# Optimization experiments

Hardware: AMD Instinct MI355X
Metric: run time of the kernel (lower is better)

Reference implementation:

```python
import jax, jax.numpy as jnp
import numpy as np

V, E, HD, K = 100000, 128, 256, 9
B, T = 128, 512
H = HD // 2  # per-direction hidden size


def setup_inputs() -> dict:
    key = jax.random.key(0)
    ks = jax.random.split(key, 16)
    s = 0.1
    rn = lambda k, shape: jax.random.normal(k, shape, jnp.float32) * s
    sentences = jax.random.randint(ks[0], (B, T), 0, V, dtype=jnp.int32)
    lengths = jax.random.randint(ks[1], (B,), 1, T + 1, dtype=jnp.int32)
    return {
        'sentences': sentences,
        'lengths': lengths,
        'embed': rn(ks[2], (V, E)),
        'Wih_f': rn(ks[3], (4 * H, E)), 'Whh_f': rn(ks[4], (4 * H, H)),
        'bih_f': rn(ks[5], (4 * H,)), 'bhh_f': rn(ks[6], (4 * H,)),
        'Wih_b': rn(ks[7], (4 * H, E)), 'Whh_b': rn(ks[8], (4 * H, H)),
        'bih_b': rn(ks[9], (4 * H,)), 'bhh_b': rn(ks[10], (4 * H,)),
        'W_out': rn(ks[11], (K, HD)), 'b_out': rn(ks[12], (K,)),
        'start_t': rn(ks[13], (K,)), 'end_t': rn(ks[14], (K,)),
        'trans': rn(ks[15], (K, K)),
    }


def _lstm(x, mask, Wih, Whh, bih, bhh, reverse):
    # x: [B,T,E], mask: [B,T] bool. Replicates packed-sequence semantics:
    # state frozen and output zeroed at padding positions (padding is trailing,
    # so reverse=True starts fresh at each sequence's true end).
    Bv, Hv = x.shape[0], Whh.shape[1]
    bias = bih + bhh

    def step(carry, inp):
        h, c = carry
        x_t, m_t = inp  # [B,E], [B,1]
        gates = x_t @ Wih.T + h @ Whh.T + bias  # [B,4H]
        i, f, g, o = jnp.split(gates, 4, axis=-1)  # torch gate order i,f,g,o
        c_new = jax.nn.sigmoid(f) * c + jax.nn.sigmoid(i) * jnp.tanh(g)
        h_new = jax.nn.sigmoid(o) * jnp.tanh(c_new)
        h = jnp.where(m_t, h_new, h)
        c = jnp.where(m_t, c_new, c)
        return (h, c), h * m_t.astype(h.dtype)

    init = (jnp.zeros((Bv, Hv), x.dtype), jnp.zeros((Bv, Hv), x.dtype))
    xs = (jnp.swapaxes(x, 0, 1), jnp.swapaxes(mask, 0, 1)[..., None])
    _, hs = jax.lax.scan(step, init, xs, reverse=reverse)
    return jnp.swapaxes(hs, 0, 1)  # [B,T,H]


def _emissions(sentences, mask, embed, Wih_f, Whh_f, bih_f, bhh_f,
               Wih_b, Whh_b, bih_b, bhh_b, W_out, b_out):
    x = embed[sentences]  # [B,T,E] (dropout is identity at inference)
    hf = _lstm(x, mask, Wih_f, Whh_f, bih_f, bhh_f, reverse=False)
    hb = _lstm(x, mask, Wih_b, Whh_b, bih_b, bhh_b, reverse=True)
    h = jnp.concatenate([hf, hb], axis=-1)  # [B,T,2H]
    return jnp.einsum('btd,kd->btk', h, W_out) + b_out  # [B,T,K]


def _viterbi(em, mask, start_t, end_t, trans):
    # torchcrf-style batched Viterbi decode. em: [B,T,K], mask: [B,T] bool.
    Kv = em.shape[-1]
    ident = jnp.arange(Kv, dtype=jnp.int32)[None]  # identity backpointers for pads
    score0 = start_t[None] + em[:, 0]  # [B,K]

    def step(score, inp):
        em_t, m_t = inp  # [B,K], [B,1]
        cand = score[:, :, None] + trans[None] + em_t[:, None, :]  # [B,K_prev,K_cur]
        new_score = cand.max(axis=1)
        idx = cand.argmax(axis=1).astype(jnp.int32)  # [B,K]
        score = jnp.where(m_t, new_score, score)
        idx = jnp.where(m_t, idx, ident)
        return score, idx

    xs = (jnp.swapaxes(em[:, 1:], 0, 1), jnp.swapaxes(mask[:, 1:], 0, 1)[..., None])
    score, hist = jax.lax.scan(step, score0, xs)  # hist: [T-1,B,K]
    score = score + end_t[None]
    last_tag = jnp.argmax(score, axis=-1).astype(jnp.int32)  # [B]

    def back(tag, idx_t):
        prev = jnp.take_along_axis(idx_t, tag[:, None], axis=1)[:, 0]
        return prev, prev

    _, tags_prev = jax.lax.scan(back, last_tag, hist, reverse=True)  # [T-1,B]
    tags = jnp.swapaxes(jnp.concatenate([tags_prev, last_tag[None]], axis=0), 0, 1)
    return jnp.where(mask, tags, 0), score.max(axis=-1)


def reference(sentences, lengths, embed, Wih_f, Whh_f, bih_f, bhh_f,
              Wih_b, Whh_b, bih_b, bhh_b, W_out, b_out, start_t, end_t, trans):
    mask = jnp.arange(sentences.shape[1])[None] < lengths[:, None]  # [B,T]
    em = _emissions(sentences, mask, embed, Wih_f, Whh_f, bih_f, bhh_f,
                    Wih_b, Whh_b, bih_b, bhh_b, W_out, b_out)
    tags, _ = _viterbi(em, mask, start_t, end_t, trans)
    return tags  # [B,T] int32, padded positions set to 0
```

## Files before the change

### kernel.cpp

```cpp
#include <hip/hip_runtime.h>
#include <cmath>

#define B_  128
#define T_  512
#define E_  128
#define H_  128
#define G4  512
#define K_  9

__global__ __launch_bounds__(256, 2)
void proj_gemm(const int* __restrict__ sent, const float* __restrict__ embed,
               const float* __restrict__ Wf, const float* __restrict__ Wb,
               const float* __restrict__ bif, const float* __restrict__ bhf,
               const float* __restrict__ bib, const float* __restrict__ bhb,
               float* __restrict__ proj, int t0f, int Tc)
{
  __shared__ __align__(16) float Al[128 * 64];
  __shared__ __align__(16) float Bl[128 * 64];
  const int tid   = threadIdx.x;
  const int ntile = blockIdx.x;
  const int mtile = blockIdx.y;
  const int tpb   = Tc >> 6;
  const int b     = mtile / tpb;
  const int toff  = (mtile - b * tpb) << 6;
  const int dir   = ntile >> 3;
  const int t0    = dir ? (T_ - t0f - Tc) : t0f;
  const float* __restrict__ W = dir ? Wb : Wf;
  const int n0 = (ntile & 7) << 6;

  {
    const int r  = tid & 63;
    const int kc = tid >> 6;
    const int t  = t0 + toff + r;
    const int vid = sent[b * T_ + t];
    const float* arow = embed + (size_t)vid * E_ + kc * 32;
    const float* brow = W + (size_t)(n0 + r) * E_ + kc * 32;
#pragma unroll
    for (int q = 0; q < 8; ++q) {
      float4 av = *(const float4*)(arow + q * 4);
      float4 bv = *(const float4*)(brow + q * 4);
      int k0 = kc * 32 + q * 4;
      Al[(k0 + 0) * 64 + r] = av.x; Al[(k0 + 1) * 64 + r] = av.y;
      Al[(k0 + 2) * 64 + r] = av.z; Al[(k0 + 3) * 64 + r] = av.w;
      Bl[(k0 + 0) * 64 + r] = bv.x; Bl[(k0 + 1) * 64 + r] = bv.y;
      Bl[(k0 + 2) * 64 + r] = bv.z; Bl[(k0 + 3) * 64 + r] = bv.w;
    }
  }
  __syncthreads();

  const int mg = tid & 15, ng = tid >> 4;
  float acc[4][4] = {};
#pragma unroll 8
  for (int k = 0; k < 128; ++k) {
    float4 a  = *(const float4*)&Al[k * 64 + mg * 4];
    float4 bb = *(const float4*)&Bl[k * 64 + ng * 4];
    acc[0][0] += a.x * bb.x; acc[0][1] += a.x * bb.y; acc[0][2] += a.x * bb.z; acc[0][3] += a.x * bb.w;
    acc[1][0] += a.y * bb.x; acc[1][1] += a.y * bb.y; acc[1][2] += a.y * bb.z; acc[1][3] += a.y * bb.w;
    acc[2][0] += a.z * bb.x; acc[2][1] += a.z * bb.y; acc[2][2] += a.z * bb.z; acc[2][3] += a.z * bb.w;
    acc[3][0] += a.w * bb.x; acc[3][1] += a.w * bb.y; acc[3][2] += a.w * bb.z; acc[3][3] += a.w * bb.w;
  }

  const float* bi = dir ? bib : bif;
  const float* bh = dir ? bhb : bhf;
  const int nl = ng * 4;
  float4 bias;
  bias.x = bi[n0 + nl + 0] + bh[n0 + nl + 0];
  bias.y = bi[n0 + nl + 1] + bh[n0 + nl + 1];
  bias.z = bi[n0 + nl + 2] + bh[n0 + nl + 2];
  bias.w = bi[n0 + nl + 3] + bh[n0 + nl + 3];
#pragma unroll
  for (int i = 0; i < 4; ++i) {
    const int tloc = toff + mg * 4 + i;
    float4 o;
    o.x = acc[i][0] + bias.x; o.y = acc[i][1] + bias.y;
    o.z = acc[i][2] + bias.z; o.w = acc[i][3] + bias.w;
    *(float4*)&proj[((size_t)(b * Tc + tloc)) * 1024 + dir * G4 + n0 + nl] = o;
  }
}

__global__ __launch_bounds__(512, 1)
void lstm_chunk(const float* __restrict__ proj,
                const float* __restrict__ Whf, const float* __restrict__ Whb,
                const int* __restrict__ lengths,
                float* __restrict__ hs,
                float* __restrict__ sh, float* __restrict__ sc,
                int t0f, int Tc, int first)
{
  const int dir = blockIdx.x;
  const int b   = blockIdx.y;
  const int tid = threadIdx.x;
  const float* __restrict__ Whh = dir ? Whb : Whf;
  __shared__ __align__(16) float h_lds[H_];
  __shared__ float gates[G4];

  float w[128];
  {
    const float* wr = Whh + (size_t)tid * H_;
#pragma unroll
    for (int k = 0; k < 128; k += 4) {
      float4 v = *(const float4*)(wr + k);
      w[k] = v.x; w[k + 1] = v.y; w[k + 2] = v.z; w[k + 3] = v.w;
    }
  }
#pragma unroll
  for (int k = 0; k < 128; ++k) asm volatile("" : "+v"(w[k]));

  const int len = lengths[b];
  const int t0  = dir ? (T_ - t0f - Tc) : t0f;
  float c = 0.f;
  if (tid < H_) {
    if (first) {
      h_lds[tid] = 0.f;
    } else {
      h_lds[tid] = sh[(dir * B_ + b) * H_ + tid];
      c          = sc[(dir * B_ + b) * H_ + tid];
    }
  }
  __syncthreads();

  const float* projp = proj + (size_t)b * Tc * 1024 + dir * G4 + tid;
  float pv = projp[(size_t)(dir ? (Tc - 1) : 0) * 1024];
  for (int s = 0; s < Tc; ++s) {
    const int tc = dir ? (Tc - 1 - s) : s;
    const int t  = t0 + tc;
    float nv = 0.f;
    if (s + 1 < Tc) {
      const int tcn = dir ? (Tc - 2 - s) : (s + 1);
      nv = projp[(size_t)tcn * 1024];
    }
    float a0 = 0.f, a1 = 0.f, a2 = 0.f, a3 = 0.f;
#pragma unroll
    for (int k4 = 0; k4 < 32; ++k4) {
      float4 h4 = *(const float4*)&h_lds[k4 * 4];
      a0 += w[4 * k4 + 0] * h4.x; a1 += w[4 * k4 + 1] * h4.y;
      a2 += w[4 * k4 + 2] * h4.z; a3 += w[4 * k4 + 3] * h4.w;
    }
    float acc = pv + (a0 + a1) + (a2 + a3);
    const int blk = tid >> 7;
    gates[tid] = (blk == 2) ? tanhf(acc) : 1.f / (1.f + expf(-acc));
    __syncthreads();
    if (tid < H_) {
      float gi = gates[tid], gf = gates[tid + 128];
      float gg = gates[tid + 256], go = gates[tid + 384];
      float cn = gf * c + gi * gg;
      float hn = go * tanhf(cn);
      bool  m  = (t < len);
      float hold = h_lds[tid];
      c = m ? cn : c;
      h_lds[tid] = m ? hn : hold;
      hs[(size_t)(b * T_ + t) * 256 + dir * H_ + tid] = m ? hn : 0.f;
    }
    __syncthreads();
    pv = nv;
  }
  if (tid < H_) {
    sh[(dir * B_ + b) * H_ + tid] = h_lds[tid];
    sc[(dir * B_ + b) * H_ + tid] = c;
  }
}

__global__ __launch_bounds__(256)
void emis_kernel(const float* __restrict__ hs, const float* __restrict__ Wout,
                 const float* __restrict__ bout, float* __restrict__ em)
{
  __shared__ __align__(16) float Wl[K_ * 256];
  const int tid = threadIdx.x;
  for (int i = tid; i < K_ * 256; i += 256) Wl[i] = Wout[i];
  __syncthreads();
  const int m = blockIdx.x * 256 + tid;
  const float* h = hs + (size_t)m * 256;
  float acc[K_] = {};
#pragma unroll 4
  for (int kk = 0; kk < 64; ++kk) {
    float4 h4 = *(const float4*)(h + kk * 4);
#pragma unroll
    for (int k9 = 0; k9 < K_; ++k9) {
      float4 w4 = *(const float4*)&Wl[k9 * 256 + kk * 4];
      acc[k9] += h4.x * w4.x + h4.y * w4.y + h4.z * w4.z + h4.w * w4.w;
    }
  }
#pragma unroll
  for (int k9 = 0; k9 < K_; ++k9) em[(size_t)m * K_ + k9] = acc[k9] + bout[k9];
}

__global__ __launch_bounds__(64)
void viterbi_kernel(const float* __restrict__ em, const int* __restrict__ lengths,
                    const float* __restrict__ st, const float* __restrict__ en,
                    const float* __restrict__ trans, int* __restrict__ tags)
{
  const int b    = blockIdx.x;
  const int lane = threadIdx.x;
  __shared__ unsigned char hist[(T_ - 1) * 16];
  const int len = lengths[b];
  float tr[K_];
#pragma unroll
  for (int j = 0; j < K_; ++j) tr[j] = (lane < K_) ? trans[j * K_ + lane] : 0.f;
  float s = (lane < K_) ? st[lane] + em[(size_t)(b * T_) * K_ + lane] : -1e30f;
  for (int t = 1; t < len; ++t) {
    float best = -1e30f; int bj = 0;
#pragma unroll
    for (int j = 0; j < K_; ++j) {
      float v = __shfl(s, j) + tr[j];
      if (v > best) { best = v; bj = j; }
    }
    if (lane < K_) {
      s = best + em[(size_t)(b * T_ + t) * K_ + lane];
      hist[(t - 1) * 16 + lane] = (unsigned char)bj;
    }
  }
  float fs = (lane < K_) ? s + en[lane] : -1e30f;
  float best = -1e30f; int last = 0;
#pragma unroll
  for (int j = 0; j < K_; ++j) {
    float v = __shfl(fs, j);
    if (v > best) { best = v; last = j; }
  }
  __syncthreads();
  if (lane == 0) {
    int tag = last;
    tags[b * T_ + len - 1] = tag;
    for (int t = len - 2; t >= 0; --t) {
      tag = hist[t * 16 + tag];
      tags[b * T_ + t] = tag;
    }
  }
  for (int t = len + lane; t < T_; t += 64) tags[b * T_ + t] = 0;
}

extern "C" void kernel_launch(void* const* d_in, const int* in_sizes, int n_in,
                              void* d_out, int out_size, void* d_ws, size_t ws_size,
                              hipStream_t stream)
{
  const int*   sent  = (const int*)d_in[0];
  const int*   lens  = (const int*)d_in[1];
  const float* embed = (const float*)d_in[2];
  const float* Wif   = (const float*)d_in[3];
  const float* Whf   = (const float*)d_in[4];
  const float* bif   = (const float*)d_in[5];
  const float* bhf   = (const float*)d_in[6];
  const float* Wib   = (const float*)d_in[7];
  const float* Whb   = (const float*)d_in[8];
  const float* bib   = (const float*)d_in[9];
  const float* bhb   = (const float*)d_in[10];
  const float* Wout  = (const float*)d_in[11];
  const float* bout  = (const float*)d_in[12];
  const float* stt   = (const float*)d_in[13];
  const float* ent   = (const float*)d_in[14];
  const float* trans = (const float*)d_in[15];
  int* tags = (int*)d_out;

  float* ws   = (float*)d_ws;
  float* hs   = ws;
  float* em   = hs + (size_t)B_ * T_ * 256;
  float* sh   = em + (size_t)B_ * T_ * K_;
  float* sc   = sh + (size_t)2 * B_ * H_;
  float* proj = sc + (size_t)2 * B_ * H_;
  const size_t fixed_bytes = (size_t)(proj - ws) * sizeof(float);

  int Tc = 512;
  while (Tc > 64 && fixed_bytes + (size_t)B_ * Tc * 1024 * sizeof(float) > ws_size)
    Tc >>= 1;

  const int nch = T_ / Tc;
  for (int c2 = 0; c2 < nch; ++c2) {
    const int t0f = c2 * Tc;
    dim3 g1(16, B_ * (Tc >> 6));
    hipLaunchKernelGGL(proj_gemm, g1, dim3(256), 0, stream,
                       sent, embed, Wif, Wib, bif, bhf, bib, bhb, proj, t0f, Tc);
    dim3 g2(2, B_);
    hipLaunchKernelGGL(lstm_chunk, g2, dim3(512), 0, stream,
                       proj, Whf, Whb, lens, hs, sh, sc, t0f, Tc, (int)(c2 == 0));
  }
  hipLaunchKernelGGL(emis_kernel, dim3((B_ * T_) / 256), dim3(256), 0, stream,
                     hs, Wout, bout, em);
  hipLaunchKernelGGL(viterbi_kernel, dim3(B_), dim3(64), 0, stream,
                     em, lens, stt, ent, trans, tags);
}
```

Measured before the change: 967.8 us.

## Enlarge projection GEMM tile to 128x128 with 8x8 micro-tiles and double-buffered K

Reworks the embedding-gather input projection GEMM to use 128x128 output tiles with an 8x8 per-thread register micro-tile. K is staged in 32-wide slices through double-buffered shared memory, with the next slice loaded into registers while the current one is computed. This raises arithmetic intensity per shared-memory load and hides global-load latency. The cost is much higher register pressure (64 accumulators) and a minimum chunk size of 128.

Measured after the change: 2.838 ms. 193% more time.

```diff
diff --git a/kernel.cpp b/kernel.cpp
--- a/kernel.cpp
+++ b/kernel.cpp
@@ -15,66 +15,99 @@
                const float* __restrict__ bib, const float* __restrict__ bhb,
                float* __restrict__ proj, int t0f, int Tc)
 {
-  __shared__ __align__(16) float Al[128 * 64];
-  __shared__ __align__(16) float Bl[128 * 64];
+  __shared__ __align__(16) float Al[2][32][128];
+  __shared__ __align__(16) float Bl[2][32][128];
   const int tid   = threadIdx.x;
   const int ntile = blockIdx.x;
   const int mtile = blockIdx.y;
-  const int tpb   = Tc >> 6;
-  const int b     = mtile / tpb;
-  const int toff  = (mtile - b * tpb) << 6;
-  const int dir   = ntile >> 3;
+  const int dir   = ntile >> 2;
+  const int n0    = (ntile & 3) << 7;
   const int t0    = dir ? (T_ - t0f - Tc) : t0f;
   const float* __restrict__ W = dir ? Wb : Wf;
-  const int n0 = (ntile & 7) << 6;
-
-  {
-    const int r  = tid & 63;
-    const int kc = tid >> 6;
-    const int t  = t0 + toff + r;
-    const int vid = sent[b * T_ + t];
-    const float* arow = embed + (size_t)vid * E_ + kc * 32;
-    const float* brow = W + (size_t)(n0 + r) * E_ + kc * 32;
-#pragma unroll
-    for (int q = 0; q < 8; ++q) {
-      float4 av = *(const float4*)(arow + q * 4);
-      float4 bv = *(const float4*)(brow + q * 4);
-      int k0 = kc * 32 + q * 4;
-      Al[(k0 + 0) * 64 + r] = av.x; Al[(k0 + 1) * 64 + r] = av.y;
-      Al[(k0 + 2) * 64 + r] = av.z; Al[(k0 + 3) * 64 + r] = av.w;
-      Bl[(k0 + 0) * 64 + r] = bv.x; Bl[(k0 + 1) * 64 + r] = bv.y;
-      Bl[(k0 + 2) * 64 + r] = bv.z; Bl[(k0 + 3) * 64 + r] = bv.w;
-    }
-  }
-  __syncthreads();
+
+  const int row = tid & 127;
+  const int kh  = (tid >> 7) << 4;
+  const int mrow0 = mtile * 128 + row;
+  const int b   = mrow0 / Tc;
+  const int tc  = mrow0 - b * Tc;
+  const int vid = sent[b * T_ + t0 + tc];
+  const float* __restrict__ arow = embed + (size_t)vid * E_ + kh;
+  const float* __restrict__ brow = W + (size_t)(n0 + row) * E_ + kh;
+
+  float4 va[4], vb[4];
+#pragma unroll
+  for (int q = 0; q < 4; ++q) {
+    va[q] = *(const float4*)(arow + q * 4);
+    vb[q] = *(const float4*)(brow + q * 4);
+  }
+#pragma unroll
+  for (int q = 0; q < 4; ++q) {
+    const int k = kh + q * 4;
+    Al[0][k + 0][row] = va[q].x; Al[0][k + 1][row] = va[q].y;
+    Al[0][k + 2][row] = va[q].z; Al[0][k + 3][row] = va[q].w;
+    Bl[0][k + 0][row] = vb[q].x; Bl[0][k + 1][row] = vb[q].y;
+    Bl[0][k + 2][row] = vb[q].z; Bl[0][k + 3][row] = vb[q].w;
+  }
 
   const int mg = tid & 15, ng = tid >> 4;
-  float acc[4][4] = {};
-#pragma unroll 8
-  for (int k = 0; k < 128; ++k) {
-    float4 a  = *(const float4*)&Al[k * 64 + mg * 4];
-    float4 bb = *(const float4*)&Bl[k * 64 + ng * 4];
-    acc[0][0] += a.x * bb.x; acc[0][1] += a.x * bb.y; acc[0][2] += a.x * bb.z; acc[0][3] += a.x * bb.w;
-    acc[1][0] += a.y * bb.x; acc[1][1] += a.y * bb.y; acc[1][2] += a.y * bb.z; acc[1][3] += a.y * bb.w;
-    acc[2][0] += a.z * bb.x; acc[2][1] += a.z * bb.y; acc[2][2] += a.z * bb.z; acc[2][3] += a.z * bb.w;
-    acc[3][0] += a.w * bb.x; acc[3][1] += a.w * bb.y; acc[3][2] += a.w * bb.z; acc[3][3] += a.w * bb.w;
+  float acc[8][8] = {};
+
+  for (int s = 0; s < 4; ++s) {
+    __syncthreads();
+    if (s < 3) {
+      const int kb = (s + 1) * 32;
+#pragma unroll
+      for (int q = 0; q < 4; ++q) {
+        va[q] = *(const float4*)(arow + kb + q * 4);
+        vb[q] = *(const float4*)(brow + kb + q * 4);
+      }
+    }
+    const int bs = s & 1;
+#pragma unroll
+    for (int k = 0; k < 32; ++k) {
+      float4 a0 = *(const float4*)&Al[bs][k][mg * 4];
+      float4 a1 = *(const float4*)&Al[bs][k][64 + mg * 4];
+      float4 b0 = *(const float4*)&Bl[bs][k][ng * 4];
+      float4 b1 = *(const float4*)&Bl[bs][k][64 + ng * 4];
+      float av[8] = {a0.x, a0.y, a0.z, a0.w, a1.x, a1.y, a1.z, a1.w};
+      float bv[8] = {b0.x, b0.y, b0.z, b0.w, b1.x, b1.y, b1.z, b1.w};
+#pragma unroll
+      for (int i = 0; i < 8; ++i)
+#pragma unroll
+        for (int j = 0; j < 8; ++j) acc[i][j] += av[i] * bv[j];
+    }
+    if (s < 3) {
+      const int nb = (s + 1) & 1;
+#pragma unroll
+      for (int q = 0; q < 4; ++q) {
+        const int k = kh + q * 4;
+        Al[nb][k + 0][row] = va[q].x; Al[nb][k + 1][row] = va[q].y;
+        Al[nb][k + 2][row] = va[q].z; Al[nb][k + 3][row] = va[q].w;
+        Bl[nb][k + 0][row] = vb[q].x; Bl[nb][k + 1][row] = vb[q].y;
+        Bl[nb][k + 2][row] = vb[q].z; Bl[nb][k + 3][row] = vb[q].w;
+      }
+    }
   }
 
   const float* bi = dir ? bib : bif;
   const float* bh = dir ? bhb : bhf;
-  const int nl = ng * 4;
-  float4 bias;
-  bias.x = bi[n0 + nl + 0] + bh[n0 + nl + 0];
-  bias.y = bi[n0 + nl + 1] + bh[n0 + nl + 1];
-  bias.z = bi[n0 + nl + 2] + bh[n0 + nl + 2];
-  bias.w = bi[n0 + nl + 3] + bh[n0 + nl + 3];
-#pragma unroll
-  for (int i = 0; i < 4; ++i) {
-    const int tloc = toff + mg * 4 + i;
-    float4 o;
-    o.x = acc[i][0] + bias.x; o.y = acc[i][1] + bias.y;
-    o.z = acc[i][2] + bias.z; o.w = acc[i][3] + bias.w;
-    *(float4*)&proj[((size_t)(b * Tc + tloc)) * 1024 + dir * G4 + n0 + nl] = o;
+  float bias[8];
+#pragma unroll
+  for (int cj = 0; cj < 8; ++cj) {
+    const int col = n0 + (cj >> 2) * 64 + ng * 4 + (cj & 3);
+    bias[cj] = bi[col] + bh[col];
+  }
+#pragma unroll
+  for (int ri = 0; ri < 8; ++ri) {
+    const int mrow = mtile * 128 + (ri >> 2) * 64 + mg * 4 + (ri & 3);
+    float* prow = proj + (size_t)mrow * 1024 + dir * G4 + n0;
+    float4 o0, o1;
+    o0.x = acc[ri][0] + bias[0]; o0.y = acc[ri][1] + bias[1];
+    o0.z = acc[ri][2] + bias[2]; o0.w = acc[ri][3] + bias[3];
+    o1.x = acc[ri][4] + bias[4]; o1.y = acc[ri][5] + bias[5];
+    o1.z = acc[ri][6] + bias[6]; o1.w = acc[ri][7] + bias[7];
+    *(float4*)&prow[ng * 4]      = o0;
+    *(float4*)&prow[64 + ng * 4] = o1;
   }
 }
 
@@ -258,13 +291,13 @@
   const size_t fixed_bytes = (size_t)(proj - ws) * sizeof(float);
 
   int Tc = 512;
-  while (Tc > 64 && fixed_bytes + (size_t)B_ * Tc * 1024 * sizeof(float) > ws_size)
+  while (Tc > 128 && fixed_bytes + (size_t)B_ * Tc * 1024 * sizeof(float) > ws_size)
     Tc >>= 1;
 
   const int nch = T_ / Tc;
   for (int c2 = 0; c2 < nch; ++c2) {
     const int t0f = c2 * Tc;
-    dim3 g1(16, B_ * (Tc >> 6));
+    dim3 g1(8, (B_ * Tc) >> 7);
     hipLaunchKernelGGL(proj_gemm, g1, dim3(256), 0, stream,
                        sent, embed, Wif, Wib, bif, bhf, bib, bhb, proj, t0f, Tc);
     dim3 g2(2, B_);
```

## Retile projection GEMM to 128x128 blocks with 8x8 register microtiles

Applied to the files above, without the earlier changes.

The input-projection GEMM moves from 64x64 output tiles with a 4x4 per-thread microtile to 128x128 tiles with an 8x8 microtile. The K dimension is staged through LDS in two halves of 64. The goal is to raise arithmetic intensity per LDS and global load and cut the number of blocks. In exchange it uses more registers per thread, drops the 2-blocks-per-CU launch bound, and requires the time chunk Tc to be at least 128.

Measured after the change: 1.059 ms. +9.5%, slower.

```diff
diff --git a/kernel.cpp b/kernel.cpp
--- a/kernel.cpp
+++ b/kernel.cpp
@@ -8,73 +8,95 @@
 #define G4  512
 #define K_  9
 
-__global__ __launch_bounds__(256, 2)
+#define MT8(L, R, A)                                              \
+  L.x += A * B0.x; L.y += A * B0.y; L.z += A * B0.z; L.w += A * B0.w; \
+  R.x += A * B1.x; R.y += A * B1.y; R.z += A * B1.z; R.w += A * B1.w;
+
+__global__ __launch_bounds__(256)
 void proj_gemm(const int* __restrict__ sent, const float* __restrict__ embed,
                const float* __restrict__ Wf, const float* __restrict__ Wb,
                const float* __restrict__ bif, const float* __restrict__ bhf,
                const float* __restrict__ bib, const float* __restrict__ bhb,
                float* __restrict__ proj, int t0f, int Tc)
 {
-  __shared__ __align__(16) float Al[128 * 64];
-  __shared__ __align__(16) float Bl[128 * 64];
+  __shared__ __align__(16) float Al[64][128];
+  __shared__ __align__(16) float Bl[64][128];
   const int tid   = threadIdx.x;
   const int ntile = blockIdx.x;
   const int mtile = blockIdx.y;
-  const int tpb   = Tc >> 6;
-  const int b     = mtile / tpb;
-  const int toff  = (mtile - b * tpb) << 6;
-  const int dir   = ntile >> 3;
+  const int dir   = ntile >> 2;
+  const int n0    = (ntile & 3) << 7;
   const int t0    = dir ? (T_ - t0f - Tc) : t0f;
   const float* __restrict__ W = dir ? Wb : Wf;
-  const int n0 = (ntile & 7) << 6;
-
-  {
-    const int r  = tid & 63;
-    const int kc = tid >> 6;
-    const int t  = t0 + toff + r;
-    const int vid = sent[b * T_ + t];
-    const float* arow = embed + (size_t)vid * E_ + kc * 32;
-    const float* brow = W + (size_t)(n0 + r) * E_ + kc * 32;
+
+  const int row   = tid & 127;
+  const int kh    = (tid >> 7) << 5;
+  const int mrow0 = mtile * 128 + row;
+  const int b     = mrow0 / Tc;
+  const int tc    = mrow0 - b * Tc;
+  const int vid   = sent[b * T_ + t0 + tc];
+  const float* __restrict__ arow = embed + (size_t)vid * E_ + kh;
+  const float* __restrict__ brow = W + (size_t)(n0 + row) * E_ + kh;
+
+  const int mg = tid & 15, ng = tid >> 4;
+  float4 accL[8] = {}, accR[8] = {};
+  for (int s = 0; s < 2; ++s) {
+    if (s) __syncthreads();
+    const int kb = s << 6;
 #pragma unroll
     for (int q = 0; q < 8; ++q) {
-      float4 av = *(const float4*)(arow + q * 4);
-      float4 bv = *(const float4*)(brow + q * 4);
-      int k0 = kc * 32 + q * 4;
-      Al[(k0 + 0) * 64 + r] = av.x; Al[(k0 + 1) * 64 + r] = av.y;
-      Al[(k0 + 2) * 64 + r] = av.z; Al[(k0 + 3) * 64 + r] = av.w;
-      Bl[(k0 + 0) * 64 + r] = bv.x; Bl[(k0 + 1) * 64 + r] = bv.y;
-      Bl[(k0 + 2) * 64 + r] = bv.z; Bl[(k0 + 3) * 64 + r] = bv.w;
-    }
-  }
-  __syncthreads();
-
-  const int mg = tid & 15, ng = tid >> 4;
-  float acc[4][4] = {};
-#pragma unroll 8
-  for (int k = 0; k < 128; ++k) {
-    float4 a  = *(const float4*)&Al[k * 64 + mg * 4];
-    float4 bb = *(const float4*)&Bl[k * 64 + ng * 4];
-    acc[0][0] += a.x * bb.x; acc[0][1] += a.x * bb.y; acc[0][2] += a.x * bb.z; acc[0][3] += a.x * bb.w;
-    acc[1][0] += a.y * bb.x; acc[1][1] += a.y * bb.y; acc[1][2] += a.y * bb.z; acc[1][3] += a.y * bb.w;
-    acc[2][0] += a.z * bb.x; acc[2][1] += a.z * bb.y; acc[2][2] += a.z * bb.z; acc[2][3] += a.z * bb.w;
-    acc[3][0] += a.w * bb.x; acc[3][1] += a.w * bb.y; acc[3][2] += a.w * bb.z; acc[3][3] += a.w * bb.w;
+      float4 v = *(const float4*)(arow + kb + q * 4);
+      const int k = kh + q * 4;
+      Al[k + 0][row] = v.x; Al[k + 1][row] = v.y;
+      Al[k + 2][row] = v.z; Al[k + 3][row] = v.w;
+    }
+#pragma unroll
+    for (int q = 0; q < 8; ++q) {
+      float4 v = *(const float4*)(brow + kb + q * 4);
+      const int k = kh + q * 4;
+      Bl[k + 0][row] = v.x; Bl[k + 1][row] = v.y;
+      Bl[k + 2][row] = v.z; Bl[k + 3][row] = v.w;
+    }
+    __syncthreads();
+#pragma unroll
+    for (int k = 0; k < 64; ++k) {
+      float4 A0 = *(const float4*)&Al[k][mg * 4];
+      float4 A1 = *(const float4*)&Al[k][64 + mg * 4];
+      float4 B0 = *(const float4*)&Bl[k][ng * 4];
+      float4 B1 = *(const float4*)&Bl[k][64 + ng * 4];
+      MT8(accL[0], accR[0], A0.x)
+      MT8(accL[1], accR[1], A0.y)
+      MT8(accL[2], accR[2], A0.z)
+      MT8(accL[3], accR[3], A0.w)
+      MT8(accL[4], accR[4], A1.x)
+      MT8(accL[5], accR[5], A1.y)
+      MT8(accL[6], accR[6], A1.z)
+      MT8(accL[7], accR[7], A1.w)
+    }
   }
 
   const float* bi = dir ? bib : bif;
   const float* bh = dir ? bhb : bhf;
-  const int nl = ng * 4;
-  float4 bias;
-  bias.x = bi[n0 + nl + 0] + bh[n0 + nl + 0];
-  bias.y = bi[n0 + nl + 1] + bh[n0 + nl + 1];
-  bias.z = bi[n0 + nl + 2] + bh[n0 + nl + 2];
-  bias.w = bi[n0 + nl + 3] + bh[n0 + nl + 3];
-#pragma unroll
-  for (int i = 0; i < 4; ++i) {
-    const int tloc = toff + mg * 4 + i;
-    float4 o;
-    o.x = acc[i][0] + bias.x; o.y = acc[i][1] + bias.y;
-    o.z = acc[i][2] + bias.z; o.w = acc[i][3] + bias.w;
-    *(float4*)&proj[((size_t)(b * Tc + tloc)) * 1024 + dir * G4 + n0 + nl] = o;
+  float4 biasL, biasR;
+  biasL.x = bi[n0 + ng * 4 + 0] + bh[n0 + ng * 4 + 0];
+  biasL.y = bi[n0 + ng * 4 + 1] + bh[n0 + ng * 4 + 1];
+  biasL.z = bi[n0 + ng * 4 + 2] + bh[n0 + ng * 4 + 2];
+  biasL.w = bi[n0 + ng * 4 + 3] + bh[n0 + ng * 4 + 3];
+  biasR.x = bi[n0 + 64 + ng * 4 + 0] + bh[n0 + 64 + ng * 4 + 0];
+  biasR.y = bi[n0 + 64 + ng * 4 + 1] + bh[n0 + 64 + ng * 4 + 1];
+  biasR.z = bi[n0 + 64 + ng * 4 + 2] + bh[n0 + 64 + ng * 4 + 2];
+  biasR.w = bi[n0 + 64 + ng * 4 + 3] + bh[n0 + 64 + ng * 4 + 3];
+#pragma unroll
+  for (int i = 0; i < 8; ++i) {
+    const int mrow = mtile * 128 + (i >> 2) * 64 + mg * 4 + (i & 3);
+    float* prow = proj + (size_t)mrow * 1024 + dir * G4 + n0;
+    float4 oL, oR;
+    oL.x = accL[i].x + biasL.x; oL.y = accL[i].y + biasL.y;
+    oL.z = accL[i].z + biasL.z; oL.w = accL[i].w + biasL.w;
+    oR.x = accR[i].x + biasR.x; oR.y = accR[i].y + biasR.y;
+    oR.z = accR[i].z + biasR.z; oR.w = accR[i].w + biasR.w;
+    *(float4*)&prow[ng * 4]      = oL;
+    *(float4*)&prow[64 + ng * 4] = oR;
   }
 }
 
@@ -258,13 +280,13 @@
   const size_t fixed_bytes = (size_t)(proj - ws) * sizeof(float);
 
   int Tc = 512;
-  while (Tc > 64 && fixed_bytes + (size_t)B_ * Tc * 1024 * sizeof(float) > ws_size)
+  while (Tc > 128 && fixed_bytes + (size_t)B_ * Tc * 1024 * sizeof(float) > ws_size)
     Tc >>= 1;
 
   const int nch = T_ / Tc;
   for (int c2 = 0; c2 < nch; ++c2) {
     const int t0f = c2 * Tc;
-    dim3 g1(16, B_ * (Tc >> 6));
+    dim3 g1(8, (B_ * Tc) >> 7);
     hipLaunchKernelGGL(proj_gemm, g1, dim3(256), 0, stream,
                        sent, embed, Wif, Wib, bif, bhf, bib, bhb, proj, t0f, Tc);
     dim3 g2(2, B_);
```
